# Kernel tuning notes

Hardware: AMD Instinct MI355X
Metric: run time of the kernel (lower is better)

The kernel has to match this reference:

```python
import jax, jax.numpy as jnp
import numpy as np

N = 2048      # feature_num (nodes/sensors)
T = 5         # timd_num (window length)
D = 64        # embed_dim
TOPK = 21     # topk + 1 (includes self, cos(i,i)=1)
B = 32        # batch
EPS = 1e-5
NEG_SLOPE = 0.2


def setup_inputs() -> dict:
    key = jax.random.key(0)
    ks = jax.random.split(key, 9)
    s = 1.0 / np.sqrt(D)
    return {
        "x": jax.random.normal(ks[0], (B, N, T), jnp.float32),
        "emb": jax.random.normal(ks[1], (N, D), jnp.float32) * s,      # embedding table
        "W": jax.random.normal(ks[2], (D, T), jnp.float32) * (1.0 / np.sqrt(T)),  # GNN lin weight
        "Wb": jax.random.normal(ks[3], (D,), jnp.float32) * 0.01,       # GNN lin bias
        "a_src": jax.random.normal(ks[4], (2 * D,), jnp.float32) * s,   # attention vec (source half)
        "a_dst": jax.random.normal(ks[5], (2 * D,), jnp.float32) * s,   # attention vec (dest half)
        "gamma": jnp.ones((D,), jnp.float32),                            # BatchNorm1d weight
        "beta": jnp.zeros((D,), jnp.float32),                            # BatchNorm1d bias
        "fc_w": jax.random.normal(ks[6], (1, D), jnp.float32) * s,      # fc weight
        "fc_b": jnp.zeros((1,), jnp.float32),                            # fc bias
    }


def reference(x, emb, W, Wb, a_src, a_dst, gamma, beta, fc_w, fc_b):
    # --- cosine-sim topk graph build ---
    norm = jnp.linalg.norm(emb, axis=-1)                    # [N]
    cos = (emb @ emb.T) / (norm[:, None] * norm[None, :])   # [N,N]
    _, idx = jax.lax.top_k(cos, TOPK)                       # [N,TOPK]
    # scatter one-hot adjacency (vectorized, no per-row loop)
    adj = jnp.zeros((N, N), x.dtype).at[jnp.arange(N)[:, None], idx].set(1.0)
    # --- GNN: GDN-style attention message passing ---
    h = jnp.einsum('bnt,dt->bnd', x, W) + Wb                # [B,N,D]
    g = jnp.concatenate([h, jnp.broadcast_to(emb, h.shape)], axis=-1)  # [B,N,2D]
    e_src = g @ a_src                                       # [B,N]
    e_dst = g @ a_dst                                       # [B,N]
    e = jax.nn.leaky_relu(e_src[:, :, None] + e_dst[:, None, :], NEG_SLOPE)  # [B,N,N]
    e = jnp.where(adj > 0, e, jnp.float32(-1e9))
    alpha = jax.nn.softmax(e, axis=-1)                      # [B,N,N], rows sum to 1 over TOPK nbrs
    z = jax.nn.relu(jnp.einsum('bij,bjd->bid', alpha, h))   # [B,N,D]
    # --- output head: z * emb, BN over channels, relu, fc ---
    out = z * emb                                           # [B,N,D]
    mean = out.mean(axis=(0, 1))                            # BN1d stats over (batch, nodes)
    var = out.var(axis=(0, 1))
    out = (out - mean) * jax.lax.rsqrt(var + EPS) * gamma + beta
    out = jax.nn.relu(out)
    out = out @ fc_w.T + fc_b                               # [B,N,1]
    return out.reshape(-1, N)                               # [B,N]
```

## Files before the change

kernel.cpp:

```cpp
#include <hip/hip_runtime.h>
#include <math.h>

#define N_NODES 2048
#define T_WIN 5
#define D_EMB 64
#define TOPK 21
#define B_BATCH 32
#define BN_TOTAL (B_BATCH * N_NODES)
#define EPS_BN 1e-5f
#define NEG_SLOPE 0.2f
#define STATS_STRIDE 16

typedef unsigned long long u64;

__device__ __forceinline__ float wave_sum(float v) {
#pragma unroll
    for (int off = 32; off > 0; off >>= 1) v += __shfl_xor(v, off, 64);
    return v;
}

__device__ __forceinline__ u64 max64(u64 a, u64 b) { return a > b ? a : b; }
__device__ __forceinline__ u64 min64(u64 a, u64 b) { return a < b ? a : b; }

__device__ __forceinline__ u64 bitonic_sort64_desc(u64 key, int lane) {
#pragma unroll
    for (int k = 2; k <= 64; k <<= 1) {
#pragma unroll
        for (int j = k >> 1; j >= 1; j >>= 1) {
            u64 pk = __shfl_xor(key, j, 64);
            bool dirDesc = ((lane & k) == 0);
            bool keepMax = (((lane & j) == 0) == dirDesc);
            key = keepMax ? max64(key, pk) : min64(key, pk);
        }
    }
    return key;
}

__device__ __forceinline__ u64 bitonic_merge_top64(u64 a, u64 b, int lane) {
    u64 br = __shfl(b, 63 - lane, 64);
    u64 c = max64(a, br);
#pragma unroll
    for (int j = 32; j >= 1; j >>= 1) {
        u64 pk = __shfl_xor(c, j, 64);
        bool keepMax = ((lane & j) == 0);
        c = keepMax ? max64(c, pk) : min64(c, pk);
    }
    return c;
}

__global__ __launch_bounds__(256) void k_edge(
    const float* __restrict__ x, const float* __restrict__ W,
    const float* __restrict__ Wb, const float* __restrict__ a_src,
    const float* __restrict__ a_dst, const float* __restrict__ emb,
    float* __restrict__ es2T, float* __restrict__ ed2T,
    float* __restrict__ norms, float* __restrict__ stats,
    float* __restrict__ stats2) {
    if (blockIdx.x < 2) {
        float* p = blockIdx.x ? stats2 : stats;
        ((float4*)p)[threadIdx.x] = make_float4(0.f, 0.f, 0.f, 0.f);
    }
    int wid = threadIdx.x >> 6, lane = threadIdx.x & 63;
    int gw = blockIdx.x * 4 + wid;
    const float* wp = W + lane * T_WIN;
    float w0 = wp[0], w1 = wp[1], w2 = wp[2], w3 = wp[3], w4 = wp[4];
    float bias = Wb[lane];
    float as = a_src[lane], asE = a_src[D_EMB + lane];
    float ad = a_dst[lane], adE = a_dst[D_EMB + lane];

    for (int node = gw; node < BN_TOTAL; node += 8192) {
        int n = node & (N_NODES - 1);
        const float* xp = x + (size_t)node * T_WIN;
        float hv = bias + xp[0] * w0 + xp[1] * w1 + xp[2] * w2 + xp[3] * w3 + xp[4] * w4;
        float e = emb[n * D_EMB + lane];
        if (node < N_NODES) {
            float s2 = wave_sum(e * e);
            if (lane == 0) norms[node] = sqrtf(s2);
        }
        float es = wave_sum(hv * as + e * asE);
        float ed = wave_sum(hv * ad + e * adE);
        if (lane == 0) {
            es2T[node] = es;
            ed2T[node] = ed;
        }
    }
}

__global__ __launch_bounds__(256) void k_gram(
    const float* __restrict__ emb, const float* __restrict__ norms,
    float* __restrict__ cosM) {
    __shared__ __align__(16) float As[64][68];
    __shared__ __align__(16) float Bs[64][68];
    int t = threadIdx.x;
    int g = blockIdx.x;
    int a = (int)((sqrtf(8.f * g + 1.f) - 1.f) * 0.5f);
    while ((a + 1) * (a + 2) / 2 <= g) a++;
    while (a * (a + 1) / 2 > g) a--;
    int bq = g - a * (a + 1) / 2;
    int i0 = a * 64, j0 = bq * 64;

    {
        int r = t >> 2, c0 = t & 3;
        const float4* srcA = (const float4*)(emb + (size_t)(i0 + r) * D_EMB);
        const float4* srcB = (const float4*)(emb + (size_t)(j0 + r) * D_EMB);
#pragma unroll
        for (int k = 0; k < 4; k++) {
            int f4 = c0 + 4 * k;
            float4 v = srcA[f4];
            int d = 4 * f4;
            As[d][r] = v.x; As[d + 1][r] = v.y; As[d + 2][r] = v.z; As[d + 3][r] = v.w;
            float4 w = srcB[f4];
            Bs[d][r] = w.x; Bs[d + 1][r] = w.y; Bs[d + 2][r] = w.z; Bs[d + 3][r] = w.w;
        }
    }
    __syncthreads();

    int ti = t & 15, tj = t >> 4;
    float acc[4][4] = {};
#pragma unroll
    for (int d = 0; d < 64; d++) {
        float4 av = *(const float4*)&As[d][4 * ti];
        float4 bv = *(const float4*)&Bs[d][4 * tj];
        acc[0][0] += av.x * bv.x; acc[0][1] += av.x * bv.y; acc[0][2] += av.x * bv.z; acc[0][3] += av.x * bv.w;
        acc[1][0] += av.y * bv.x; acc[1][1] += av.y * bv.y; acc[1][2] += av.y * bv.z; acc[1][3] += av.y * bv.w;
        acc[2][0] += av.z * bv.x; acc[2][1] += av.z * bv.y; acc[2][2] += av.z * bv.z; acc[2][3] += av.z * bv.w;
        acc[3][0] += av.w * bv.x; acc[3][1] += av.w * bv.y; acc[3][2] += av.w * bv.z; acc[3][3] += av.w * bv.w;
    }

    float nis[4] = {norms[i0 + 4 * ti], norms[i0 + 4 * ti + 1],
                    norms[i0 + 4 * ti + 2], norms[i0 + 4 * ti + 3]};
    float njs[4] = {norms[j0 + 4 * tj], norms[j0 + 4 * tj + 1],
                    norms[j0 + 4 * tj + 2], norms[j0 + 4 * tj + 3]};
#pragma unroll
    for (int r = 0; r < 4; r++) {
        float4 o;
        o.x = acc[r][0] / (nis[r] * njs[0]);
        o.y = acc[r][1] / (nis[r] * njs[1]);
        o.z = acc[r][2] / (nis[r] * njs[2]);
        o.w = acc[r][3] / (nis[r] * njs[3]);
        int i = i0 + 4 * ti + r;
        *(float4*)(cosM + (size_t)i * N_NODES + j0 + 4 * tj) = o;
        cosM[(size_t)(j0 + 4 * tj + 0) * N_NODES + i] = o.x;
        cosM[(size_t)(j0 + 4 * tj + 1) * N_NODES + i] = o.y;
        cosM[(size_t)(j0 + 4 * tj + 2) * N_NODES + i] = o.z;
        cosM[(size_t)(j0 + 4 * tj + 3) * N_NODES + i] = o.w;
    }
}

__global__ __launch_bounds__(256) void k_select(
    const float* __restrict__ cosM, int* __restrict__ idxT) {
    __shared__ u64 candbuf[4][128];
    int tid = threadIdx.x;
    int wid = tid >> 6, lane = tid & 63;
    int i = blockIdx.x * 4 + wid;
    const float* row = cosM + (size_t)i * N_NODES;
    u64* buf = candbuf[wid];

    u64 a = 0;
    u64 t = 0;
    int cnt = 0;
    float vcur = row[lane];

#pragma unroll 1
    for (int c = 0; c < N_NODES / 64; c++) {
        int j = c * 64 + lane;
        float v = vcur;
        if (c < N_NODES / 64 - 1) vcur = row[j + 64];
        unsigned u = __float_as_uint(v);
        u = (u & 0x80000000u) ? ~u : (u | 0x80000000u);
        u64 key = ((u64)u << 32) | (unsigned)(~j);
        unsigned long long ball = __ballot(key > t);
        if (ball) {
            int ofs = __popcll(ball & ((1ull << lane) - 1ull));
            if (key > t) buf[cnt + ofs] = key;
            cnt += (int)__popcll(ball);
            if (cnt >= 64) {
                u64 nk = buf[lane];
                nk = bitonic_sort64_desc(nk, lane);
                a = bitonic_merge_top64(a, nk, lane);
                t = __shfl(a, 20, 64);
                int rem = cnt - 64;
                u64 mv = (lane < rem) ? buf[64 + lane] : 0;
                if (lane < rem) buf[lane] = mv;
                cnt = rem;
            }
        }
    }
    while (cnt > 0) {
        int take = cnt < 64 ? cnt : 64;
        u64 nk = (lane < take) ? buf[lane] : 0;
        nk = bitonic_sort64_desc(nk, lane);
        a = bitonic_merge_top64(a, nk, lane);
        t = __shfl(a, 20, 64);
        int rem = cnt - take;
        u64 mv = (lane < rem) ? buf[take + lane] : 0;
        if (lane < rem) buf[lane] = mv;
        cnt = rem;
    }

    if (lane < TOPK) idxT[lane * N_NODES + i] = (int)(~(unsigned)a);
}

__global__ __launch_bounds__(256) void k_alpha(
    const int* __restrict__ idxT, const float* __restrict__ es2T,
    const float* __restrict__ ed2T, float* __restrict__ alphaT) {
    __shared__ float sed[N_NODES];
    int g = blockIdx.x;
    int b = g & 31;
    int i0 = (g >> 5) * 256;
    int t = threadIdx.x;

    {
        const float4* src = (const float4*)(ed2T + (size_t)b * N_NODES);
        float4* dst = (float4*)sed;
#pragma unroll
        for (int q = 0; q < 2; q++) dst[t + 256 * q] = src[t + 256 * q];
    }
    __syncthreads();

    int i = i0 + t;
    float es = es2T[(size_t)b * N_NODES + i];
    float ev[TOPK];
    float m = -3e38f;
#pragma unroll
    for (int k = 0; k < TOPK; k++) {
        int jk = idxT[k * N_NODES + i];
        float e = es + sed[jk];
        e = e > 0.f ? e : NEG_SLOPE * e;
        ev[k] = e;
        m = fmaxf(m, e);
    }
    float s = 0.f;
#pragma unroll
    for (int k = 0; k < TOPK; k++) {
        ev[k] = __expf(ev[k] - m);
        s += ev[k];
    }
    float inv = 1.0f / s;
#pragma unroll
    for (int k = 0; k < TOPK; k++)
        alphaT[((size_t)b * TOPK + k) * N_NODES + i] = ev[k] * inv;
}

__global__ __launch_bounds__(256, 2) void k_msg(
    const float* __restrict__ x, const float* __restrict__ W,
    const float* __restrict__ Wb, const int* __restrict__ idxT,
    const float* __restrict__ alphaT, const float* __restrict__ emb,
    float* __restrict__ obufT, float* __restrict__ stats,
    float* __restrict__ stats2) {
    __shared__ float hts[N_NODES][6];
    __shared__ float sred[2][4][4];

    int g = blockIdx.x;
    int b = (g & 7) + 8 * ((g >> 3) & 3);
    int c = g >> 5;
    int d0 = c * 4;
    int t = threadIdx.x;
    int wid = t >> 6, lane = t & 63;

    float wc[4][T_WIN], wb4[4];
#pragma unroll
    for (int q = 0; q < 4; q++) {
        wb4[q] = Wb[d0 + q];
#pragma unroll
        for (int tt = 0; tt < T_WIN; tt++) wc[q][tt] = W[(d0 + q) * T_WIN + tt];
    }
    const float* xb = x + (size_t)b * N_NODES * T_WIN;
#pragma unroll
    for (int r = 0; r < 8; r++) {
        int row = t + 256 * r;
        const float* xr = xb + row * T_WIN;
        float x0 = xr[0], x1 = xr[1], x2 = xr[2], x3 = xr[3], x4 = xr[4];
        float h0 = wb4[0] + x0 * wc[0][0] + x1 * wc[0][1] + x2 * wc[0][2] + x3 * wc[0][3] + x4 * wc[0][4];
        float h1 = wb4[1] + x0 * wc[1][0] + x1 * wc[1][1] + x2 * wc[1][2] + x3 * wc[1][3] + x4 * wc[1][4];
        float h2 = wb4[2] + x0 * wc[2][0] + x1 * wc[2][1] + x2 * wc[2][2] + x3 * wc[2][3] + x4 * wc[2][4];
        float h3 = wb4[3] + x0 * wc[3][0] + x1 * wc[3][1] + x2 * wc[3][2] + x3 * wc[3][3] + x4 * wc[3][4];
        *(float2*)&hts[row][0] = make_float2(h0, h1);
        *(float2*)&hts[row][2] = make_float2(h2, h3);
    }
    __syncthreads();

    float sacc[4] = {0.f, 0.f, 0.f, 0.f};
    float sacc2[4] = {0.f, 0.f, 0.f, 0.f};
    const float* aT = alphaT + (size_t)b * TOPK * N_NODES;
#pragma unroll 1
    for (int r = 0; r < 8; r++) {
        int i = 256 * r + t;
        float4 z = make_float4(0.f, 0.f, 0.f, 0.f);
#pragma unroll
        for (int k = 0; k < TOPK; k++) {
            int jk = idxT[k * N_NODES + i];
            float a = aT[(size_t)k * N_NODES + i];
            float2 h01 = *(const float2*)&hts[jk][0];
            float2 h23 = *(const float2*)&hts[jk][2];
            z.x = fmaf(a, h01.x, z.x);
            z.y = fmaf(a, h01.y, z.y);
            z.z = fmaf(a, h23.x, z.z);
            z.w = fmaf(a, h23.y, z.w);
        }
        float4 e4 = *(const float4*)(emb + (size_t)i * D_EMB + d0);
        float4 o;
        o.x = fmaxf(z.x, 0.f) * e4.x;
        o.y = fmaxf(z.y, 0.f) * e4.y;
        o.z = fmaxf(z.z, 0.f) * e4.z;
        o.w = fmaxf(z.w, 0.f) * e4.w;
        ((float4*)obufT)[((size_t)c * B_BATCH + b) * N_NODES + i] = o;
        sacc[0] += o.x; sacc[1] += o.y; sacc[2] += o.z; sacc[3] += o.w;
        sacc2[0] += o.x * o.x; sacc2[1] += o.y * o.y;
        sacc2[2] += o.z * o.z; sacc2[3] += o.w * o.w;
    }

#pragma unroll
    for (int q = 0; q < 4; q++) {
        sacc[q] = wave_sum(sacc[q]);
        sacc2[q] = wave_sum(sacc2[q]);
    }
    if (lane == 0) {
#pragma unroll
        for (int q = 0; q < 4; q++) {
            sred[0][wid][q] = sacc[q];
            sred[1][wid][q] = sacc2[q];
        }
    }
    __syncthreads();
    if (t < 8) {
        int q = t & 3, which = t >> 2;
        float v = sred[which][0][q] + sred[which][1][q] + sred[which][2][q] + sred[which][3][q];
        float* dst = which ? stats2 : stats;
        atomicAdd(&dst[(d0 + q) * STATS_STRIDE], v);
    }
}

__global__ __launch_bounds__(256) void k_out(
    const float* __restrict__ obufT, const float* __restrict__ stats,
    const float* __restrict__ stats2, const float* __restrict__ gamma,
    const float* __restrict__ beta, const float* __restrict__ fc_w,
    const float* __restrict__ fc_b, float* __restrict__ out) {
    __shared__ float smean[64], sinv[64], sg[64], sb[64], sf[64];
    int t = threadIdx.x;
    int g = blockIdx.x;
    int b = g & 31, nc = g >> 5;
    int n = nc * 256 + t;
    const float invM = 1.0f / (float)BN_TOTAL;

    if (t < 64) {
        float mn = stats[t * STATS_STRIDE] * invM;
        float var = stats2[t * STATS_STRIDE] * invM - mn * mn;
        smean[t] = mn;
        sinv[t] = rsqrtf(var + EPS_BN);
        sg[t] = gamma[t]; sb[t] = beta[t]; sf[t] = fc_w[t];
    }
    __syncthreads();

    float fb = fc_b[0];
    float p = 0.f;
#pragma unroll
    for (int c = 0; c < 16; c++) {
        float4 o = ((const float4*)obufT)[((size_t)c * B_BATCH + b) * N_NODES + n];
        int d = 4 * c;
        float v;
        v = fmaxf((o.x - smean[d + 0]) * sinv[d + 0] * sg[d + 0] + sb[d + 0], 0.f); p = fmaf(v, sf[d + 0], p);
        v = fmaxf((o.y - smean[d + 1]) * sinv[d + 1] * sg[d + 1] + sb[d + 1], 0.f); p = fmaf(v, sf[d + 1], p);
        v = fmaxf((o.z - smean[d + 2]) * sinv[d + 2] * sg[d + 2] + sb[d + 2], 0.f); p = fmaf(v, sf[d + 2], p);
        v = fmaxf((o.w - smean[d + 3]) * sinv[d + 3] * sg[d + 3] + sb[d + 3], 0.f); p = fmaf(v, sf[d + 3], p);
    }
    out[b * N_NODES + n] = p + fb;
}

extern "C" void kernel_launch(void* const* d_in, const int* in_sizes, int n_in,
                              void* d_out, int out_size, void* d_ws, size_t ws_size,
                              hipStream_t stream) {
    const float* x     = (const float*)d_in[0];
    const float* emb   = (const float*)d_in[1];
    const float* W     = (const float*)d_in[2];
    const float* Wb    = (const float*)d_in[3];
    const float* a_src = (const float*)d_in[4];
    const float* a_dst = (const float*)d_in[5];
    const float* gamma = (const float*)d_in[6];
    const float* beta  = (const float*)d_in[7];
    const float* fc_w  = (const float*)d_in[8];
    const float* fc_b  = (const float*)d_in[9];
    float* out = (float*)d_out;

    char* ws = (char*)d_ws;
    float* stats  = (float*)(ws + 0);
    float* stats2 = (float*)(ws + 4096);
    int*   idxT   = (int*)  (ws + 8192);
    float* norms  = (float*)(ws + 180224);
    float* es2T   = (float*)(ws + 188416);
    float* ed2T   = (float*)(ws + 450560);
    float* alphaT = (float*)(ws + 712704);
    float* cosM   = (float*)(ws + 6217728);
    float* obufT  = cosM;

    k_edge<<<2048, 256, 0, stream>>>(x, W, Wb, a_src, a_dst, emb,
                                     es2T, ed2T, norms, stats, stats2);
    k_gram<<<528, 256, 0, stream>>>(emb, norms, cosM);
    k_select<<<N_NODES / 4, 256, 0, stream>>>(cosM, idxT);
    k_alpha<<<256, 256, 0, stream>>>(idxT, es2T, ed2T, alphaT);
    k_msg<<<512, 256, 0, stream>>>(x, W, Wb, idxT, alphaT, emb, obufT, stats, stats2);
    k_out<<<256, 256, 0, stream>>>(obufT, stats, stats2, gamma, beta, fc_w, fc_b, out);
}
```

Baseline: 147.4 us.

## Merge edge and gram kernels; pack alpha with neighbor index

Fuses the edge-score kernel and the gram kernel into a single launch. The gram blocks now write raw dot products, and the cosine normalization moves into the top-k select loop, which removes the gram kernel's dependency on norms. The alpha kernel writes (alpha, index) pairs interleaved as float2, so the message kernel does one 8-byte load per neighbor instead of two separate 4-byte loads. In exchange, the edge work runs on fewer blocks with a longer loop, and the select loop does an extra norm load and a division per element.

```diff
diff --git a/kernel.cpp b/kernel.cpp
--- a/kernel.cpp
+++ b/kernel.cpp
@@ -48,46 +48,46 @@
     return c;
 }
 
-__global__ __launch_bounds__(256) void k_edge(
+__global__ __launch_bounds__(256) void k_pre(
     const float* __restrict__ x, const float* __restrict__ W,
     const float* __restrict__ Wb, const float* __restrict__ a_src,
     const float* __restrict__ a_dst, const float* __restrict__ emb,
     float* __restrict__ es2T, float* __restrict__ ed2T,
-    float* __restrict__ norms, float* __restrict__ stats,
-    float* __restrict__ stats2) {
-    if (blockIdx.x < 2) {
-        float* p = blockIdx.x ? stats2 : stats;
-        ((float4*)p)[threadIdx.x] = make_float4(0.f, 0.f, 0.f, 0.f);
-    }
-    int wid = threadIdx.x >> 6, lane = threadIdx.x & 63;
-    int gw = blockIdx.x * 4 + wid;
-    const float* wp = W + lane * T_WIN;
-    float w0 = wp[0], w1 = wp[1], w2 = wp[2], w3 = wp[3], w4 = wp[4];
-    float bias = Wb[lane];
-    float as = a_src[lane], asE = a_src[D_EMB + lane];
-    float ad = a_dst[lane], adE = a_dst[D_EMB + lane];
-
-    for (int node = gw; node < BN_TOTAL; node += 8192) {
-        int n = node & (N_NODES - 1);
-        const float* xp = x + (size_t)node * T_WIN;
-        float hv = bias + xp[0] * w0 + xp[1] * w1 + xp[2] * w2 + xp[3] * w3 + xp[4] * w4;
-        float e = emb[n * D_EMB + lane];
-        if (node < N_NODES) {
-            float s2 = wave_sum(e * e);
-            if (lane == 0) norms[node] = sqrtf(s2);
-        }
-        float es = wave_sum(hv * as + e * asE);
-        float ed = wave_sum(hv * ad + e * adE);
-        if (lane == 0) {
-            es2T[node] = es;
-            ed2T[node] = ed;
-        }
-    }
-}
-
-__global__ __launch_bounds__(256) void k_gram(
-    const float* __restrict__ emb, const float* __restrict__ norms,
-    float* __restrict__ cosM) {
+    float* __restrict__ norms, float* __restrict__ dotM,
+    float* __restrict__ stats, float* __restrict__ stats2) {
+    if (blockIdx.x >= 528) {
+        int eb = blockIdx.x - 528;
+        if (eb < 2) {
+            float* p = eb ? stats2 : stats;
+            ((float4*)p)[threadIdx.x] = make_float4(0.f, 0.f, 0.f, 0.f);
+        }
+        int wid = threadIdx.x >> 6, lane = threadIdx.x & 63;
+        int gw = eb * 4 + wid;
+        const float* wp = W + lane * T_WIN;
+        float w0 = wp[0], w1 = wp[1], w2 = wp[2], w3 = wp[3], w4 = wp[4];
+        float bias = Wb[lane];
+        float as = a_src[lane], asE = a_src[D_EMB + lane];
+        float ad = a_dst[lane], adE = a_dst[D_EMB + lane];
+
+        for (int node = gw; node < BN_TOTAL; node += 1024) {
+            int n = node & (N_NODES - 1);
+            const float* xp = x + (size_t)node * T_WIN;
+            float hv = bias + xp[0] * w0 + xp[1] * w1 + xp[2] * w2 + xp[3] * w3 + xp[4] * w4;
+            float e = emb[n * D_EMB + lane];
+            if (node < N_NODES) {
+                float s2 = wave_sum(e * e);
+                if (lane == 0) norms[node] = sqrtf(s2);
+            }
+            float es = wave_sum(hv * as + e * asE);
+            float ed = wave_sum(hv * ad + e * adE);
+            if (lane == 0) {
+                es2T[node] = es;
+                ed2T[node] = ed;
+            }
+        }
+        return;
+    }
+
     __shared__ __align__(16) float As[64][68];
     __shared__ __align__(16) float Bs[64][68];
     int t = threadIdx.x;
@@ -126,45 +126,42 @@
         acc[3][0] += av.w * bv.x; acc[3][1] += av.w * bv.y; acc[3][2] += av.w * bv.z; acc[3][3] += av.w * bv.w;
     }
 
-    float nis[4] = {norms[i0 + 4 * ti], norms[i0 + 4 * ti + 1],
-                    norms[i0 + 4 * ti + 2], norms[i0 + 4 * ti + 3]};
-    float njs[4] = {norms[j0 + 4 * tj], norms[j0 + 4 * tj + 1],
-                    norms[j0 + 4 * tj + 2], norms[j0 + 4 * tj + 3]};
 #pragma unroll
     for (int r = 0; r < 4; r++) {
         float4 o;
-        o.x = acc[r][0] / (nis[r] * njs[0]);
-        o.y = acc[r][1] / (nis[r] * njs[1]);
-        o.z = acc[r][2] / (nis[r] * njs[2]);
-        o.w = acc[r][3] / (nis[r] * njs[3]);
+        o.x = acc[r][0]; o.y = acc[r][1]; o.z = acc[r][2]; o.w = acc[r][3];
         int i = i0 + 4 * ti + r;
-        *(float4*)(cosM + (size_t)i * N_NODES + j0 + 4 * tj) = o;
-        cosM[(size_t)(j0 + 4 * tj + 0) * N_NODES + i] = o.x;
-        cosM[(size_t)(j0 + 4 * tj + 1) * N_NODES + i] = o.y;
-        cosM[(size_t)(j0 + 4 * tj + 2) * N_NODES + i] = o.z;
-        cosM[(size_t)(j0 + 4 * tj + 3) * N_NODES + i] = o.w;
+        *(float4*)(dotM + (size_t)i * N_NODES + j0 + 4 * tj) = o;
+        dotM[(size_t)(j0 + 4 * tj + 0) * N_NODES + i] = o.x;
+        dotM[(size_t)(j0 + 4 * tj + 1) * N_NODES + i] = o.y;
+        dotM[(size_t)(j0 + 4 * tj + 2) * N_NODES + i] = o.z;
+        dotM[(size_t)(j0 + 4 * tj + 3) * N_NODES + i] = o.w;
     }
 }
 
 __global__ __launch_bounds__(256) void k_select(
-    const float* __restrict__ cosM, int* __restrict__ idxT) {
+    const float* __restrict__ dotM, const float* __restrict__ norms,
+    int* __restrict__ idxT) {
     __shared__ u64 candbuf[4][128];
     int tid = threadIdx.x;
     int wid = tid >> 6, lane = tid & 63;
     int i = blockIdx.x * 4 + wid;
-    const float* row = cosM + (size_t)i * N_NODES;
+    const float* row = dotM + (size_t)i * N_NODES;
     u64* buf = candbuf[wid];
+    float ni = norms[i];
 
     u64 a = 0;
     u64 t = 0;
     int cnt = 0;
     float vcur = row[lane];
+    float ncur = norms[lane];
 
 #pragma unroll 1
     for (int c = 0; c < N_NODES / 64; c++) {
         int j = c * 64 + lane;
-        float v = vcur;
-        if (c < N_NODES / 64 - 1) vcur = row[j + 64];
+        float dv = vcur, nv = ncur;
+        if (c < N_NODES / 64 - 1) { vcur = row[j + 64]; ncur = norms[j + 64]; }
+        float v = dv / (ni * nv);
         unsigned u = __float_as_uint(v);
         u = (u & 0x80000000u) ? ~u : (u | 0x80000000u);
         u64 key = ((u64)u << 32) | (unsigned)(~j);
@@ -202,7 +199,7 @@
 
 __global__ __launch_bounds__(256) void k_alpha(
     const int* __restrict__ idxT, const float* __restrict__ es2T,
-    const float* __restrict__ ed2T, float* __restrict__ alphaT) {
+    const float* __restrict__ ed2T, float2* __restrict__ paT) {
     __shared__ float sed[N_NODES];
     int g = blockIdx.x;
     int b = g & 31;
@@ -219,12 +216,13 @@
 
     int i = i0 + t;
     float es = es2T[(size_t)b * N_NODES + i];
+    int jk[TOPK];
     float ev[TOPK];
     float m = -3e38f;
 #pragma unroll
     for (int k = 0; k < TOPK; k++) {
-        int jk = idxT[k * N_NODES + i];
-        float e = es + sed[jk];
+        jk[k] = idxT[k * N_NODES + i];
+        float e = es + sed[jk[k]];
         e = e > 0.f ? e : NEG_SLOPE * e;
         ev[k] = e;
         m = fmaxf(m, e);
@@ -237,16 +235,19 @@
     }
     float inv = 1.0f / s;
 #pragma unroll
-    for (int k = 0; k < TOPK; k++)
-        alphaT[((size_t)b * TOPK + k) * N_NODES + i] = ev[k] * inv;
+    for (int k = 0; k < TOPK; k++) {
+        float2 v;
+        v.x = ev[k] * inv;
+        v.y = __int_as_float(jk[k]);
+        paT[((size_t)b * TOPK + k) * N_NODES + i] = v;
+    }
 }
 
 __global__ __launch_bounds__(256, 2) void k_msg(
     const float* __restrict__ x, const float* __restrict__ W,
-    const float* __restrict__ Wb, const int* __restrict__ idxT,
-    const float* __restrict__ alphaT, const float* __restrict__ emb,
-    float* __restrict__ obufT, float* __restrict__ stats,
-    float* __restrict__ stats2) {
+    const float* __restrict__ Wb, const float2* __restrict__ paT,
+    const float* __restrict__ emb, float* __restrict__ obufT,
+    float* __restrict__ stats, float* __restrict__ stats2) {
     __shared__ float hts[N_NODES][6];
     __shared__ float sred[2][4][4];
 
@@ -281,15 +282,16 @@
 
     float sacc[4] = {0.f, 0.f, 0.f, 0.f};
     float sacc2[4] = {0.f, 0.f, 0.f, 0.f};
-    const float* aT = alphaT + (size_t)b * TOPK * N_NODES;
+    const float2* pb = paT + (size_t)b * TOPK * N_NODES;
 #pragma unroll 1
     for (int r = 0; r < 8; r++) {
         int i = 256 * r + t;
         float4 z = make_float4(0.f, 0.f, 0.f, 0.f);
 #pragma unroll
         for (int k = 0; k < TOPK; k++) {
-            int jk = idxT[k * N_NODES + i];
-            float a = aT[(size_t)k * N_NODES + i];
+            float2 pa = pb[(size_t)k * N_NODES + i];
+            int jk = __float_as_int(pa.y);
+            float a = pa.x;
             float2 h01 = *(const float2*)&hts[jk][0];
             float2 h23 = *(const float2*)&hts[jk][2];
             z.x = fmaf(a, h01.x, z.x);
@@ -382,21 +384,20 @@
     float* out = (float*)d_out;
 
     char* ws = (char*)d_ws;
-    float* stats  = (float*)(ws + 0);
-    float* stats2 = (float*)(ws + 4096);
-    int*   idxT   = (int*)  (ws + 8192);
-    float* norms  = (float*)(ws + 180224);
-    float* es2T   = (float*)(ws + 188416);
-    float* ed2T   = (float*)(ws + 450560);
-    float* alphaT = (float*)(ws + 712704);
-    float* cosM   = (float*)(ws + 6217728);
-    float* obufT  = cosM;
-
-    k_edge<<<2048, 256, 0, stream>>>(x, W, Wb, a_src, a_dst, emb,
-                                     es2T, ed2T, norms, stats, stats2);
-    k_gram<<<528, 256, 0, stream>>>(emb, norms, cosM);
-    k_select<<<N_NODES / 4, 256, 0, stream>>>(cosM, idxT);
-    k_alpha<<<256, 256, 0, stream>>>(idxT, es2T, ed2T, alphaT);
-    k_msg<<<512, 256, 0, stream>>>(x, W, Wb, idxT, alphaT, emb, obufT, stats, stats2);
+    float*  stats  = (float*) (ws + 0);
+    float*  stats2 = (float*) (ws + 4096);
+    int*    idxT   = (int*)   (ws + 8192);
+    float*  norms  = (float*) (ws + 180224);
+    float*  es2T   = (float*) (ws + 188416);
+    float*  ed2T   = (float*) (ws + 450560);
+    float2* paT    = (float2*)(ws + 712704);
+    float*  dotM   = (float*) (ws + 11722752);
+    float*  obufT  = dotM;
+
+    k_pre<<<784, 256, 0, stream>>>(x, W, Wb, a_src, a_dst, emb,
+                                   es2T, ed2T, norms, dotM, stats, stats2);
+    k_select<<<N_NODES / 4, 256, 0, stream>>>(dotM, norms, idxT);
+    k_alpha<<<256, 256, 0, stream>>>(idxT, es2T, ed2T, paT);
+    k_msg<<<512, 256, 0, stream>>>(x, W, Wb, paT, emb, obufT, stats, stats2);
     k_out<<<256, 256, 0, stream>>>(obufT, stats, stats2, gamma, beta, fc_w, fc_b, out);
 }
```

Result: slower. 171.0 us (+16.0%).
